# Optimization experiments

Measured on AMD Instinct MI355X. Metric: run time of the kernel, lower is better.

Reference implementation:

```python
import jax, jax.numpy as jnp
import numpy as np

B, C, H, W = 4, 256, 64, 64
EMB = C // 8  # embedding_channels = inChannels // k


def _conv1x1(x, w, b):
    # x: [B, Cin, H, W], w: [Cout, Cin], b: [Cout] -> [B, Cout, H, W]
    return jnp.einsum('oi,bihw->bohw', w, x) + b[None, :, None, None]


def setup_inputs() -> dict:
    key = jax.random.key(0)
    ks = jax.random.split(key, 10)
    s = 0.05
    return {
        'x': jax.random.normal(ks[0], (B, C, H, W), dtype=jnp.float32),
        'key_w': jax.random.normal(ks[1], (EMB, C), dtype=jnp.float32) * s,
        'key_b': jax.random.normal(ks[2], (EMB,), dtype=jnp.float32) * s,
        'query_w': jax.random.normal(ks[3], (EMB, C), dtype=jnp.float32) * s,
        'query_b': jax.random.normal(ks[4], (EMB,), dtype=jnp.float32) * s,
        'value_w': jax.random.normal(ks[5], (EMB, C), dtype=jnp.float32) * s,
        'value_b': jax.random.normal(ks[6], (EMB,), dtype=jnp.float32) * s,
        'att_w': jax.random.normal(ks[7], (C, EMB), dtype=jnp.float32) * s,
        'att_b': jax.random.normal(ks[8], (C,), dtype=jnp.float32) * s,
        'gamma': jnp.zeros((), dtype=jnp.float32),
    }


def reference(x, key_w, key_b, query_w, query_b, value_w, value_b, att_w, att_b, gamma):
    b, c, h, w = x.shape
    n = h * w
    f = _conv1x1(x, key_w, key_b).reshape(b, -1, n)    # [B, E, N]
    g = _conv1x1(x, query_w, query_b).reshape(b, -1, n)  # [B, E, N]
    hh = _conv1x1(x, value_w, value_b).reshape(b, -1, n)  # [B, E, N]
    # s[b,i,j] = sum_e f[b,e,i] * g[b,e,j]
    s = jnp.einsum('bei,bej->bij', f, g)  # [B, N, N]
    # NOTE: softmax over dim=1 (the i / key-index axis), NOT the last dim
    beta = jax.nn.softmax(s, axis=1)
    v = jnp.einsum('bei,bij->bej', hh, beta).reshape(b, -1, h, w)  # [B, E, H, W]
    o = _conv1x1(v, att_w, att_b)  # [B, C, H, W]
    y = gamma * o + x
    return (y, o)
```

## Files before the change

kernel.cpp:

```cpp
#include <hip/hip_runtime.h>
#include <hip/hip_bf16.h>
#include <math.h>

#define BB 4
#define CC 256
#define NN 4096
#define EE 32

typedef __attribute__((ext_vector_type(8))) short bf16x8;
typedef __attribute__((ext_vector_type(4))) float f32x4;

__device__ inline unsigned short f2bf(float x) {
    union { __hip_bfloat16 h; unsigned short u; } cv;
    cv.h = __float2bfloat16(x);
    return cv.u;
}
__device__ inline unsigned pk2(float lo, float hi) {
    return ((unsigned)f2bf(hi) << 16) | (unsigned)f2bf(lo);
}

__global__ __launch_bounds__(256) void wcvt_kernel(
    const float* __restrict__ kw, const float* __restrict__ kb,
    const float* __restrict__ qw, const float* __restrict__ qb,
    const float* __restrict__ vw, const float* __restrict__ vb,
    __hip_bfloat16* __restrict__ wB, float* __restrict__ bB)
{
    int r = blockIdx.x;
    int t = threadIdx.x;
    int rr = r & 31;
    const float* src; float scale = 1.f;
    if (r < 32)      src = kw;
    else if (r < 64) { src = qw; scale = 1.44269504f; }
    else             src = vw;
    if (t < 64) {
        float4 v = *(const float4*)(src + rr * 256 + t * 4);
        uint2 p;
        p.x = pk2(v.x * scale, v.y * scale);
        p.y = pk2(v.z * scale, v.w * scale);
        *(uint2*)((unsigned short*)wB + r * 256 + t * 4) = p;
    }
    if (r == 0 && t >= 64 && t < 160) {
        int e = t - 64;
        const float* bs = (e < 32) ? kb : ((e < 64) ? qb : vb);
        float sc = (e >= 32 && e < 64) ? 1.44269504f : 1.f;
        bB[e] = bs[e & 31] * sc;
    }
}

__global__ __launch_bounds__(256) void proj_kernel(
    const float* __restrict__ x,
    const __hip_bfloat16* __restrict__ wB, const float* __restrict__ bB,
    __hip_bfloat16* __restrict__ fT, __hip_bfloat16* __restrict__ gT,
    __hip_bfloat16* __restrict__ hT)
{
    __shared__ unsigned xs[32][132];
    int b     = blockIdx.x >> 7;
    int ibase = (blockIdx.x & 127) << 5;
    int wv    = threadIdx.x >> 6;
    int l     = threadIdx.x & 63;
    int il    = l & 31;
    int pg    = (wv << 1) | (l >> 5);

    const float* xb = x + (size_t)b * CC * NN + ibase + il;
#pragma unroll
    for (int j = 0; j < 16; ++j) {
        int p = pg + (j << 3);
        float lo = xb[(size_t)(2 * p) * NN];
        float hi = xb[(size_t)(2 * p + 1) * NN];
        xs[il][p] = pk2(lo, hi);
    }
    __syncthreads();

    int q15  = l & 15, g = l >> 4;
    int isub = wv & 1, eh = wv >> 1;
    int irow = (isub << 4) + q15;
    const __hip_bfloat16* w0 = wB + ((size_t)(eh * 48) + q15) * 256;

    f32x4 a0 = {0,0,0,0}, a1 = {0,0,0,0}, a2 = {0,0,0,0};
#pragma unroll
    for (int kk = 0; kk < 8; ++kk) {
        bf16x8 Bf = *(const bf16x8*)&xs[irow][kk * 16 + 4 * g];
        int co = kk * 32 + 8 * g;
        bf16x8 A0 = *(const bf16x8*)(w0 + co);
        bf16x8 A1 = *(const bf16x8*)(w0 + 16 * 256 + co);
        bf16x8 A2 = *(const bf16x8*)(w0 + 32 * 256 + co);
        a0 = __builtin_amdgcn_mfma_f32_16x16x32_bf16(A0, Bf, a0, 0, 0, 0);
        a1 = __builtin_amdgcn_mfma_f32_16x16x32_bf16(A1, Bf, a1, 0, 0, 0);
        a2 = __builtin_amdgcn_mfma_f32_16x16x32_bf16(A2, Bf, a2, 0, 0, 0);
    }

    int ig = ibase + irow;
    auto emit = [&](f32x4 acc, int T) {
        float4 bb = *(const float4*)(bB + T * 16 + 4 * g);
        float d0 = acc[0] + bb.x, d1 = acc[1] + bb.y;
        float d2 = acc[2] + bb.z, d3 = acc[3] + bb.w;
        if (T < 4) {
            __hip_bfloat16* dst = (T < 2) ? fT : gT;
            int eoff = ((T & 1) << 4) + 4 * g;
            uint2 pq; pq.x = pk2(d0, d1); pq.y = pk2(d2, d3);
            *(uint2*)((unsigned short*)dst + ((size_t)b * NN + ig) * EE + eoff) = pq;
        } else {
            unsigned short* dst = (unsigned short*)hT;
            int e = ((T - 4) << 4) + 4 * g;
            size_t base = ((size_t)b * EE + e) * NN + ig;
            dst[base]          = f2bf(d0);
            dst[base + NN]     = f2bf(d1);
            dst[base + 2 * NN] = f2bf(d2);
            dst[base + 3 * NN] = f2bf(d3);
        }
    };
    emit(a0, eh * 3 + 0);
    emit(a1, eh * 3 + 1);
    emit(a2, eh * 3 + 2);
}

__global__ __launch_bounds__(512) void attn_kernel(
    const __hip_bfloat16* __restrict__ fT,
    const __hip_bfloat16* __restrict__ gT,
    const __hip_bfloat16* __restrict__ hT,
    float* __restrict__ vT)
{
    int b     = blockIdx.x >> 7;
    int qbase = (blockIdx.x & 127) * 32;
    int wv    = threadIdx.x >> 6;
    int lane  = threadIdx.x & 63;
    int q15   = lane & 15;
    int g     = lane >> 4;

    const __hip_bfloat16* fb = fT + (size_t)b * NN * EE;
    const __hip_bfloat16* gb = gT + (size_t)b * NN * EE;
    const __hip_bfloat16* hb = hT + (size_t)b * EE * NN;

    bf16x8 Qf0 = *(const bf16x8*)(gb + (size_t)(qbase + q15) * EE + 8 * g);
    bf16x8 Qf1 = *(const bf16x8*)(gb + (size_t)(qbase + 16 + q15) * EE + 8 * g);

    const __hip_bfloat16* v0p = hb + (size_t)q15 * NN;
    const __hip_bfloat16* v1p = hb + (size_t)(16 + q15) * NN;

    float m0 = -1e30f, l0 = 0.f, m1 = -1e30f, l1 = 0.f;
    f32x4 O00 = {0,0,0,0}, O01 = {0,0,0,0};
    f32x4 O10 = {0,0,0,0}, O11 = {0,0,0,0};
    const f32x4 z4 = {0,0,0,0};

    int srcA = q15 + ((g & 1) << 5);
    int srcB = srcA + 16;
    bool lopair = (g < 2);

    auto sm_pv = [&](const f32x4& sa, const f32x4& sb, float& m, float& l,
                     f32x4& Oa, f32x4& Ob, const bf16x8& Vf0, const bf16x8& Vf1) {
        float mx = fmaxf(fmaxf(fmaxf(sa[0], sa[1]), fmaxf(sa[2], sa[3])),
                         fmaxf(fmaxf(sb[0], sb[1]), fmaxf(sb[2], sb[3])));
        mx = fmaxf(mx, __shfl_xor(mx, 16, 64));
        mx = fmaxf(mx, __shfl_xor(mx, 32, 64));
        if (!__all(mx <= m + 8.f)) {
            float mn   = fmaxf(m, mx);
            float corr = exp2f(m - mn);
            l *= corr; Oa *= corr; Ob *= corr;
            m = mn;
        }
        float p0 = exp2f(sa[0] - m), p1 = exp2f(sa[1] - m);
        float p2 = exp2f(sa[2] - m), p3 = exp2f(sa[3] - m);
        float p4 = exp2f(sb[0] - m), p5 = exp2f(sb[1] - m);
        float p6 = exp2f(sb[2] - m), p7 = exp2f(sb[3] - m);
        l += (p0 + p1 + p2 + p3) + (p4 + p5 + p6 + p7);

        unsigned c0 = pk2(p0, p1), c1 = pk2(p2, p3);
        unsigned d0 = pk2(p4, p5), d1 = pk2(p6, p7);
        unsigned tc0 = __shfl(c0, srcA, 64), tc1 = __shfl(c1, srcA, 64);
        unsigned tc2 = __shfl(c0, srcB, 64), tc3 = __shfl(c1, srcB, 64);
        unsigned td0 = __shfl(d0, srcA, 64), td1 = __shfl(d1, srcA, 64);
        unsigned td2 = __shfl(d0, srcB, 64), td3 = __shfl(d1, srcB, 64);
        union { unsigned u[4]; bf16x8 v; } pf;
        pf.u[0] = lopair ? tc0 : td0;
        pf.u[1] = lopair ? tc1 : td1;
        pf.u[2] = lopair ? tc2 : td2;
        pf.u[3] = lopair ? tc3 : td3;

        Oa = __builtin_amdgcn_mfma_f32_16x16x32_bf16(Vf0, pf.v, Oa, 0, 0, 0);
        Ob = __builtin_amdgcn_mfma_f32_16x16x32_bf16(Vf1, pf.v, Ob, 0, 0, 0);
    };

    int k0 = wv * 512;
    bf16x8 K0 = *(const bf16x8*)(fb + (size_t)(k0 + q15) * EE + 8 * g);
    bf16x8 K1 = *(const bf16x8*)(fb + (size_t)(k0 + 16 + q15) * EE + 8 * g);
    bf16x8 V0 = *(const bf16x8*)(v0p + k0 + 8 * g);
    bf16x8 V1 = *(const bf16x8*)(v1p + k0 + 8 * g);

    for (int c = 0; c < 16; ++c) {
        int kn = k0 + 32;
        bf16x8 nK0 = *(const bf16x8*)(fb + (size_t)(kn + q15) * EE + 8 * g);
        bf16x8 nK1 = *(const bf16x8*)(fb + (size_t)(kn + 16 + q15) * EE + 8 * g);
        bf16x8 nV0 = *(const bf16x8*)(v0p + kn + 8 * g);
        bf16x8 nV1 = *(const bf16x8*)(v1p + kn + 8 * g);

        f32x4 s00 = __builtin_amdgcn_mfma_f32_16x16x32_bf16(K0, Qf0, z4, 0, 0, 0);
        f32x4 s01 = __builtin_amdgcn_mfma_f32_16x16x32_bf16(K1, Qf0, z4, 0, 0, 0);
        f32x4 s10 = __builtin_amdgcn_mfma_f32_16x16x32_bf16(K0, Qf1, z4, 0, 0, 0);
        f32x4 s11 = __builtin_amdgcn_mfma_f32_16x16x32_bf16(K1, Qf1, z4, 0, 0, 0);

        sm_pv(s00, s01, m0, l0, O00, O01, V0, V1);
        sm_pv(s10, s11, m1, l1, O10, O11, V0, V1);

        K0 = nK0; K1 = nK1; V0 = nV0; V1 = nV1;
        k0 = kn;
    }

    __shared__ float sm[8][64][2];
    __shared__ float sl[8][64][2];
    __shared__ float so[8][64][2][8];
    sm[wv][lane][0] = m0;  sm[wv][lane][1] = m1;
    sl[wv][lane][0] = l0;  sl[wv][lane][1] = l1;
#pragma unroll
    for (int r = 0; r < 4; ++r) {
        so[wv][lane][0][r] = O00[r]; so[wv][lane][0][4 + r] = O01[r];
        so[wv][lane][1][r] = O10[r]; so[wv][lane][1][4 + r] = O11[r];
    }
    __syncthreads();

    if (wv < 2) {
        int qg = wv;
        float M = -1e30f;
#pragma unroll
        for (int w = 0; w < 8; ++w) M = fmaxf(M, sm[w][lane][qg]);
        float L = 0.f;
        float Of[8];
#pragma unroll
        for (int r = 0; r < 8; ++r) Of[r] = 0.f;
#pragma unroll
        for (int w = 0; w < 8; ++w) {
            float cw = exp2f(sm[w][lane][qg] - M);
            L += cw * sl[w][lane][qg];
#pragma unroll
            for (int r = 0; r < 8; ++r) Of[r] += cw * so[w][lane][qg][r];
        }
        L += __shfl_xor(L, 16, 64);
        L += __shfl_xor(L, 32, 64);
        float inv = 1.f / L;
        float* vp = vT + ((size_t)b * NN + qbase + 16 * qg + q15) * EE;
        f32x4 o0, o1;
#pragma unroll
        for (int r = 0; r < 4; ++r) { o0[r] = Of[r] * inv; o1[r] = Of[4 + r] * inv; }
        *(f32x4*)(vp + 4 * g) = o0;
        *(f32x4*)(vp + 16 + 4 * g) = o1;
    }
}

__global__ __launch_bounds__(256) void out_kernel(
    const float* __restrict__ vT, const float* __restrict__ aw,
    const float* __restrict__ ab, const float* __restrict__ x,
    const float* __restrict__ gamma_p,
    float* __restrict__ y, float* __restrict__ o)
{
    int blk    = blockIdx.x;
    int csplit = blk & 15;
    int itile  = (blk >> 4) & 15;
    int b      = blk >> 8;
    int i      = itile * 256 + threadIdx.x;
    float gm   = gamma_p[0];

    const float4* vp4 = (const float4*)(vT + ((size_t)b * NN + i) * EE);
    float vr[EE];
#pragma unroll
    for (int u = 0; u < 8; ++u) {
        float4 t = vp4[u];
        vr[4*u+0] = t.x; vr[4*u+1] = t.y; vr[4*u+2] = t.z; vr[4*u+3] = t.w;
    }

    int co0 = csplit * 16;
#pragma unroll
    for (int co = co0; co < co0 + 16; ++co) {
        float s = ab[co];
#pragma unroll
        for (int e = 0; e < EE; ++e)
            s = fmaf(aw[co * EE + e], vr[e], s);
        size_t idx = ((size_t)b * CC + co) * NN + i;
        o[idx] = s;
        y[idx] = fmaf(gm, s, x[idx]);
    }
}

extern "C" void kernel_launch(void* const* d_in, const int* in_sizes, int n_in,
                              void* d_out, int out_size, void* d_ws, size_t ws_size,
                              hipStream_t stream)
{
    const float* x  = (const float*)d_in[0];
    const float* kw = (const float*)d_in[1];
    const float* kb = (const float*)d_in[2];
    const float* qw = (const float*)d_in[3];
    const float* qb = (const float*)d_in[4];
    const float* vw = (const float*)d_in[5];
    const float* vb = (const float*)d_in[6];
    const float* aw = (const float*)d_in[7];
    const float* ab = (const float*)d_in[8];
    const float* gm = (const float*)d_in[9];

    float* y = (float*)d_out;
    float* o = y + (size_t)BB * CC * NN;

    float*          vT = (float*)d_ws;
    float*          bB = vT + (size_t)BB * NN * EE;
    __hip_bfloat16* wB = (__hip_bfloat16*)(bB + 128);
    __hip_bfloat16* fT = wB + 96 * 256;
    __hip_bfloat16* gT = fT + (size_t)BB * NN * EE;
    __hip_bfloat16* hT = gT + (size_t)BB * NN * EE;

    wcvt_kernel<<<96, 256, 0, stream>>>(kw, kb, qw, qb, vw, vb, wB, bB);
    proj_kernel<<<BB * (NN / 32), 256, 0, stream>>>(x, wB, bB, fT, gT, hT);
    attn_kernel<<<BB * (NN / 32), 512, 0, stream>>>(fT, gT, hT, vT);
    out_kernel<<<BB * 16 * 16, 256, 0, stream>>>(vT, aw, ab, x, gm, y, o);
}
```

Measured before the change: 68.98 us.

## Switch attention kernel to 32x32x16 MFMA with permlane32 swap for P layout

Rewrites the flash-attention inner loop to use 32x32x16 bf16 MFMA tiles instead of four 16x16x32 tiles, so each wave computes a 32x32 score block with one accumulator. The P matrix is converted to the B-operand layout with permlane32_swap instead of eight cross-lane shuffles and selects, and the row max needs one fewer shuffle. The final cross-wave reduction is simplified to a single wave with a padded shared array. This aims to cut shuffle/ALU overhead per tile, at the risk of a longer MFMA latency chain and higher register pressure.

```diff
diff --git a/kernel.cpp b/kernel.cpp
--- a/kernel.cpp
+++ b/kernel.cpp
@@ -9,6 +9,8 @@
 
 typedef __attribute__((ext_vector_type(8))) short bf16x8;
 typedef __attribute__((ext_vector_type(4))) float f32x4;
+typedef __attribute__((ext_vector_type(16))) float f32x16;
+typedef __attribute__((ext_vector_type(2))) unsigned uint32x2_t;
 
 __device__ inline unsigned short f2bf(float x) {
     union { __hip_bfloat16 h; unsigned short u; } cv;
@@ -124,124 +126,112 @@
     int qbase = (blockIdx.x & 127) * 32;
     int wv    = threadIdx.x >> 6;
     int lane  = threadIdx.x & 63;
-    int q15   = lane & 15;
-    int g     = lane >> 4;
+    int q     = lane & 31;
+    int h     = lane >> 5;
 
     const __hip_bfloat16* fb = fT + (size_t)b * NN * EE;
     const __hip_bfloat16* gb = gT + (size_t)b * NN * EE;
-    const __hip_bfloat16* hb = hT + (size_t)b * EE * NN;
-
-    bf16x8 Qf0 = *(const bf16x8*)(gb + (size_t)(qbase + q15) * EE + 8 * g);
-    bf16x8 Qf1 = *(const bf16x8*)(gb + (size_t)(qbase + 16 + q15) * EE + 8 * g);
-
-    const __hip_bfloat16* v0p = hb + (size_t)q15 * NN;
-    const __hip_bfloat16* v1p = hb + (size_t)(16 + q15) * NN;
-
-    float m0 = -1e30f, l0 = 0.f, m1 = -1e30f, l1 = 0.f;
-    f32x4 O00 = {0,0,0,0}, O01 = {0,0,0,0};
-    f32x4 O10 = {0,0,0,0}, O11 = {0,0,0,0};
-    const f32x4 z4 = {0,0,0,0};
-
-    int srcA = q15 + ((g & 1) << 5);
-    int srcB = srcA + 16;
-    bool lopair = (g < 2);
-
-    auto sm_pv = [&](const f32x4& sa, const f32x4& sb, float& m, float& l,
-                     f32x4& Oa, f32x4& Ob, const bf16x8& Vf0, const bf16x8& Vf1) {
-        float mx = fmaxf(fmaxf(fmaxf(sa[0], sa[1]), fmaxf(sa[2], sa[3])),
-                         fmaxf(fmaxf(sb[0], sb[1]), fmaxf(sb[2], sb[3])));
-        mx = fmaxf(mx, __shfl_xor(mx, 16, 64));
+    const __hip_bfloat16* hb = hT + (size_t)b * EE * NN + (size_t)q * NN;
+
+    bf16x8 Qf0 = *(const bf16x8*)(gb + (size_t)(qbase + q) * EE + 8 * h);
+    bf16x8 Qf1 = *(const bf16x8*)(gb + (size_t)(qbase + q) * EE + 16 + 8 * h);
+
+    float m = -1e30f, l = 0.f;
+    f32x16 O = {0,0,0,0,0,0,0,0,0,0,0,0,0,0,0,0};
+    const f32x16 z16 = {0,0,0,0,0,0,0,0,0,0,0,0,0,0,0,0};
+
+    int k0 = wv * 512;
+    bf16x8 K0 = *(const bf16x8*)(fb + (size_t)(k0 + q) * EE + 8 * h);
+    bf16x8 K1 = *(const bf16x8*)(fb + (size_t)(k0 + q) * EE + 16 + 8 * h);
+    bf16x8 V0 = *(const bf16x8*)(hb + k0 + 8 * h);
+    bf16x8 V1 = *(const bf16x8*)(hb + k0 + 16 + 8 * h);
+
+    for (int c = 0; c < 16; ++c) {
+        int kn = (k0 + 32) & (NN - 1);
+        bf16x8 nK0 = *(const bf16x8*)(fb + (size_t)(kn + q) * EE + 8 * h);
+        bf16x8 nK1 = *(const bf16x8*)(fb + (size_t)(kn + q) * EE + 16 + 8 * h);
+        bf16x8 nV0 = *(const bf16x8*)(hb + kn + 8 * h);
+        bf16x8 nV1 = *(const bf16x8*)(hb + kn + 16 + 8 * h);
+
+        f32x16 S = __builtin_amdgcn_mfma_f32_32x32x16_bf16(K0, Qf0, z16, 0, 0, 0);
+        S = __builtin_amdgcn_mfma_f32_32x32x16_bf16(K1, Qf1, S, 0, 0, 0);
+
+        float x0 = fmaxf(fmaxf(S[0], S[1]),  fmaxf(S[2], S[3]));
+        float x1 = fmaxf(fmaxf(S[4], S[5]),  fmaxf(S[6], S[7]));
+        float x2 = fmaxf(fmaxf(S[8], S[9]),  fmaxf(S[10], S[11]));
+        float x3 = fmaxf(fmaxf(S[12], S[13]), fmaxf(S[14], S[15]));
+        float mx = fmaxf(fmaxf(x0, x1), fmaxf(x2, x3));
         mx = fmaxf(mx, __shfl_xor(mx, 32, 64));
         if (!__all(mx <= m + 8.f)) {
             float mn   = fmaxf(m, mx);
             float corr = exp2f(m - mn);
-            l *= corr; Oa *= corr; Ob *= corr;
+            l *= corr;  O *= corr;
             m = mn;
         }
-        float p0 = exp2f(sa[0] - m), p1 = exp2f(sa[1] - m);
-        float p2 = exp2f(sa[2] - m), p3 = exp2f(sa[3] - m);
-        float p4 = exp2f(sb[0] - m), p5 = exp2f(sb[1] - m);
-        float p6 = exp2f(sb[2] - m), p7 = exp2f(sb[3] - m);
-        l += (p0 + p1 + p2 + p3) + (p4 + p5 + p6 + p7);
-
-        unsigned c0 = pk2(p0, p1), c1 = pk2(p2, p3);
-        unsigned d0 = pk2(p4, p5), d1 = pk2(p6, p7);
-        unsigned tc0 = __shfl(c0, srcA, 64), tc1 = __shfl(c1, srcA, 64);
-        unsigned tc2 = __shfl(c0, srcB, 64), tc3 = __shfl(c1, srcB, 64);
-        unsigned td0 = __shfl(d0, srcA, 64), td1 = __shfl(d1, srcA, 64);
-        unsigned td2 = __shfl(d0, srcB, 64), td3 = __shfl(d1, srcB, 64);
-        union { unsigned u[4]; bf16x8 v; } pf;
-        pf.u[0] = lopair ? tc0 : td0;
-        pf.u[1] = lopair ? tc1 : td1;
-        pf.u[2] = lopair ? tc2 : td2;
-        pf.u[3] = lopair ? tc3 : td3;
-
-        Oa = __builtin_amdgcn_mfma_f32_16x16x32_bf16(Vf0, pf.v, Oa, 0, 0, 0);
-        Ob = __builtin_amdgcn_mfma_f32_16x16x32_bf16(Vf1, pf.v, Ob, 0, 0, 0);
-    };
-
-    int k0 = wv * 512;
-    bf16x8 K0 = *(const bf16x8*)(fb + (size_t)(k0 + q15) * EE + 8 * g);
-    bf16x8 K1 = *(const bf16x8*)(fb + (size_t)(k0 + 16 + q15) * EE + 8 * g);
-    bf16x8 V0 = *(const bf16x8*)(v0p + k0 + 8 * g);
-    bf16x8 V1 = *(const bf16x8*)(v1p + k0 + 8 * g);
-
-    for (int c = 0; c < 16; ++c) {
-        int kn = k0 + 32;
-        bf16x8 nK0 = *(const bf16x8*)(fb + (size_t)(kn + q15) * EE + 8 * g);
-        bf16x8 nK1 = *(const bf16x8*)(fb + (size_t)(kn + 16 + q15) * EE + 8 * g);
-        bf16x8 nV0 = *(const bf16x8*)(v0p + kn + 8 * g);
-        bf16x8 nV1 = *(const bf16x8*)(v1p + kn + 8 * g);
-
-        f32x4 s00 = __builtin_amdgcn_mfma_f32_16x16x32_bf16(K0, Qf0, z4, 0, 0, 0);
-        f32x4 s01 = __builtin_amdgcn_mfma_f32_16x16x32_bf16(K1, Qf0, z4, 0, 0, 0);
-        f32x4 s10 = __builtin_amdgcn_mfma_f32_16x16x32_bf16(K0, Qf1, z4, 0, 0, 0);
-        f32x4 s11 = __builtin_amdgcn_mfma_f32_16x16x32_bf16(K1, Qf1, z4, 0, 0, 0);
-
-        sm_pv(s00, s01, m0, l0, O00, O01, V0, V1);
-        sm_pv(s10, s11, m1, l1, O10, O11, V0, V1);
+        float p[16];
+#pragma unroll
+        for (int r = 0; r < 16; ++r) p[r] = exp2f(S[r] - m);
+        float s0 = (p[0] + p[1]) + (p[2] + p[3]);
+        float s1 = (p[4] + p[5]) + (p[6] + p[7]);
+        float s2 = (p[8] + p[9]) + (p[10] + p[11]);
+        float s3 = (p[12] + p[13]) + (p[14] + p[15]);
+        l += (s0 + s1) + (s2 + s3);
+
+        unsigned j0 = pk2(p[0], p[1]),   j1 = pk2(p[2], p[3]);
+        unsigned j2 = pk2(p[4], p[5]),   j3 = pk2(p[6], p[7]);
+        unsigned j4 = pk2(p[8], p[9]),   j5 = pk2(p[10], p[11]);
+        unsigned j6 = pk2(p[12], p[13]), j7 = pk2(p[14], p[15]);
+
+        uint32x2_t sA = __builtin_amdgcn_permlane32_swap(j0, j2, false, false);
+        uint32x2_t sB = __builtin_amdgcn_permlane32_swap(j1, j3, false, false);
+        union { unsigned u[4]; bf16x8 v; } P1;
+        P1.u[0] = sA.x; P1.u[1] = sB.x; P1.u[2] = sA.y; P1.u[3] = sB.y;
+        uint32x2_t sC = __builtin_amdgcn_permlane32_swap(j4, j6, false, false);
+        uint32x2_t sD = __builtin_amdgcn_permlane32_swap(j5, j7, false, false);
+        union { unsigned u[4]; bf16x8 v; } P2;
+        P2.u[0] = sC.x; P2.u[1] = sD.x; P2.u[2] = sC.y; P2.u[3] = sD.y;
+
+        O = __builtin_amdgcn_mfma_f32_32x32x16_bf16(V0, P1.v, O, 0, 0, 0);
+        O = __builtin_amdgcn_mfma_f32_32x32x16_bf16(V1, P2.v, O, 0, 0, 0);
 
         K0 = nK0; K1 = nK1; V0 = nV0; V1 = nV1;
-        k0 = kn;
-    }
-
-    __shared__ float sm[8][64][2];
-    __shared__ float sl[8][64][2];
-    __shared__ float so[8][64][2][8];
-    sm[wv][lane][0] = m0;  sm[wv][lane][1] = m1;
-    sl[wv][lane][0] = l0;  sl[wv][lane][1] = l1;
-#pragma unroll
-    for (int r = 0; r < 4; ++r) {
-        so[wv][lane][0][r] = O00[r]; so[wv][lane][0][4 + r] = O01[r];
-        so[wv][lane][1][r] = O10[r]; so[wv][lane][1][4 + r] = O11[r];
-    }
+        k0 += 32;
+    }
+
+    __shared__ float smx[8][64];
+    __shared__ float slx[8][64];
+    __shared__ float sO[8][64][17];
+    smx[wv][lane] = m;
+    slx[wv][lane] = l;
+#pragma unroll
+    for (int r = 0; r < 16; ++r) sO[wv][lane][r] = O[r];
     __syncthreads();
 
-    if (wv < 2) {
-        int qg = wv;
-        float M = -1e30f;
-#pragma unroll
-        for (int w = 0; w < 8; ++w) M = fmaxf(M, sm[w][lane][qg]);
+    if (wv == 0) {
+        float M = smx[0][lane];
+#pragma unroll
+        for (int w = 1; w < 8; ++w) M = fmaxf(M, smx[w][lane]);
         float L = 0.f;
-        float Of[8];
-#pragma unroll
-        for (int r = 0; r < 8; ++r) Of[r] = 0.f;
+        float Of[16];
+#pragma unroll
+        for (int r = 0; r < 16; ++r) Of[r] = 0.f;
 #pragma unroll
         for (int w = 0; w < 8; ++w) {
-            float cw = exp2f(sm[w][lane][qg] - M);
-            L += cw * sl[w][lane][qg];
-#pragma unroll
-            for (int r = 0; r < 8; ++r) Of[r] += cw * so[w][lane][qg][r];
+            float cw = exp2f(smx[w][lane] - M);
+            L += cw * slx[w][lane];
+#pragma unroll
+            for (int r = 0; r < 16; ++r) Of[r] += cw * sO[w][lane][r];
         }
-        L += __shfl_xor(L, 16, 64);
         L += __shfl_xor(L, 32, 64);
         float inv = 1.f / L;
-        float* vp = vT + ((size_t)b * NN + qbase + 16 * qg + q15) * EE;
-        f32x4 o0, o1;
-#pragma unroll
-        for (int r = 0; r < 4; ++r) { o0[r] = Of[r] * inv; o1[r] = Of[4 + r] * inv; }
-        *(f32x4*)(vp + 4 * g) = o0;
-        *(f32x4*)(vp + 16 + 4 * g) = o1;
+        float* vp = vT + ((size_t)b * NN + qbase + q) * EE;
+#pragma unroll
+        for (int gi = 0; gi < 4; ++gi) {
+            f32x4 ov;
+#pragma unroll
+            for (int r = 0; r < 4; ++r) ov[r] = Of[4 * gi + r] * inv;
+            *(f32x4*)(vp + 8 * gi + 4 * h) = ov;
+        }
     }
 }
 
```

Result: faster. 64.24 us (-6.9%).
